# Kernel optimization log

Hardware: AMD Instinct MI355X
Metric: run time of the kernel (lower is better)

## Reference

```python
import jax, jax.numpy as jnp
import numpy as np

EPS = 1e-4  # matches torch: x.norm(2, dim=1, keepdim=True) + 0.0001

def setup_inputs() -> dict:
    key = jax.random.key(0)
    k1, k2, k3 = jax.random.split(key, 3)
    B, IN, OUT = 16384, 2048, 2048
    x = jax.random.normal(k1, (B, IN), dtype=jnp.float32)
    # nn.Linear default init: U(-1/sqrt(in), 1/sqrt(in))
    bound = 1.0 / np.sqrt(IN)
    W = jax.random.uniform(k2, (OUT, IN), dtype=jnp.float32, minval=-bound, maxval=bound)
    b = jax.random.uniform(k3, (OUT,), dtype=jnp.float32, minval=-bound, maxval=bound)
    return {"x": x, "W": W, "b": b}

def reference(x, W, b):
    # L2-normalize each row, then Linear, then ReLU
    norm = jnp.linalg.norm(x, ord=2, axis=1, keepdims=True)  # [B, 1]
    x_dir = x / (norm + EPS)
    h = jnp.einsum('bi,oi->bo', x_dir, W) + b  # [B, OUT]
    return jax.nn.relu(h)
```

## Files before the change

kernel.cpp:

```cpp
#include <hip/hip_runtime.h>
#include <hip/hip_bf16.h>
#include <stdint.h>

#define B_ROWS 16384
#define IN_DIM 2048
#define OUT_DIM 2048

typedef __attribute__((ext_vector_type(4))) float f32x4;
typedef __attribute__((ext_vector_type(8))) short s16x8;

__device__ __forceinline__ unsigned short f2bf_rne(float f) {
  union { float f; unsigned u; } c; c.f = f;
  unsigned u = c.u;
  return (unsigned short)((u + 0x7FFFu + ((u >> 16) & 1u)) >> 16);
}

__global__ void __launch_bounds__(256) prep_x_kernel(const float* __restrict__ x,
                                                     unsigned short* __restrict__ xn,
                                                     float* __restrict__ scale) {
  const int row = blockIdx.x;
  const int t = threadIdx.x;
  const float4* xr = (const float4*)(x + (size_t)row * IN_DIM);
  float4 v0 = xr[t * 2 + 0];
  float4 v1 = xr[t * 2 + 1];
  float ss = v0.x * v0.x + v0.y * v0.y + v0.z * v0.z + v0.w * v0.w +
             v1.x * v1.x + v1.y * v1.y + v1.z * v1.z + v1.w * v1.w;
  s16x8 p;
  p[0] = (short)f2bf_rne(v0.x); p[1] = (short)f2bf_rne(v0.y);
  p[2] = (short)f2bf_rne(v0.z); p[3] = (short)f2bf_rne(v0.w);
  p[4] = (short)f2bf_rne(v1.x); p[5] = (short)f2bf_rne(v1.y);
  p[6] = (short)f2bf_rne(v1.z); p[7] = (short)f2bf_rne(v1.w);
  *(s16x8*)(xn + (size_t)row * IN_DIM + t * 8) = p;

  #pragma unroll
  for (int off = 32; off > 0; off >>= 1) ss += __shfl_down(ss, off, 64);
  __shared__ float red[4];
  if ((t & 63) == 0) red[t >> 6] = ss;
  __syncthreads();
  if (t == 0) {
    float s = red[0] + red[1] + red[2] + red[3];
    scale[row] = 1.0f / (sqrtf(s) + 1e-4f);
  }
}

__global__ void __launch_bounds__(256) prep_w_kernel(const float* __restrict__ W,
                                                     unsigned short* __restrict__ Wb) {
  const size_t base = (size_t)blockIdx.x * 2048 + (size_t)threadIdx.x * 8;
  const float4* wp = (const float4*)(W + base);
  float4 v0 = wp[0];
  float4 v1 = wp[1];
  s16x8 p;
  p[0] = (short)f2bf_rne(v0.x); p[1] = (short)f2bf_rne(v0.y);
  p[2] = (short)f2bf_rne(v0.z); p[3] = (short)f2bf_rne(v0.w);
  p[4] = (short)f2bf_rne(v1.x); p[5] = (short)f2bf_rne(v1.y);
  p[6] = (short)f2bf_rne(v1.z); p[7] = (short)f2bf_rne(v1.w);
  *(s16x8*)(Wb + base) = p;
}

__global__ void __launch_bounds__(256) gemm_kernel(const unsigned short* __restrict__ A,
                                                   const unsigned short* __restrict__ Bm,
                                                   const float* __restrict__ scale,
                                                   const float* __restrict__ bias,
                                                   float* __restrict__ out) {
  constexpr int BK = 64;
  __shared__ short As[128 * BK];
  __shared__ short Bs[128 * BK];

  const int tid  = threadIdx.x;
  const int bn   = blockIdx.x;
  const int bm   = blockIdx.y;
  const int lane = tid & 63;
  const int wave = tid >> 6;
  const int wm   = wave >> 1;
  const int wn   = wave & 1;
  const int lrow = lane & 15;
  const int lq   = lane >> 4;

  const int ar = tid >> 3;
  const int ac = (tid & 7) * 8;
  const unsigned short* ag = A  + (size_t)(bm * 128 + ar) * IN_DIM + ac;
  const unsigned short* bg = Bm + (size_t)(bn * 128 + ar) * IN_DIM + ac;
  char* asl = (char*)As + tid * 16;
  char* bsl = (char*)Bs + tid * 16;

  f32x4 acc[4][4] = {};

  for (int k0 = 0; k0 < IN_DIM; k0 += BK) {
    #pragma unroll
    for (int i = 0; i < 4; ++i) {
      __builtin_amdgcn_global_load_lds(
          (const __attribute__((address_space(1))) unsigned int*)(ag + (size_t)i * 32 * IN_DIM),
          (__attribute__((address_space(3))) unsigned int*)(asl + i * 4096), 16, 0, 0);
    }
    #pragma unroll
    for (int i = 0; i < 4; ++i) {
      __builtin_amdgcn_global_load_lds(
          (const __attribute__((address_space(1))) unsigned int*)(bg + (size_t)i * 32 * IN_DIM),
          (__attribute__((address_space(3))) unsigned int*)(bsl + i * 4096), 16, 0, 0);
    }
    ag += BK;
    bg += BK;
    __syncthreads();

    #pragma unroll
    for (int kk = 0; kk < 2; ++kk) {
      s16x8 af[4], bf[4];
      #pragma unroll
      for (int mi = 0; mi < 4; ++mi)
        af[mi] = *(const s16x8*)(As + (wm * 64 + mi * 16 + lrow) * BK + kk * 32 + lq * 8);
      #pragma unroll
      for (int ni = 0; ni < 4; ++ni)
        bf[ni] = *(const s16x8*)(Bs + (wn * 64 + ni * 16 + lrow) * BK + kk * 32 + lq * 8);
      #pragma unroll
      for (int mi = 0; mi < 4; ++mi)
        #pragma unroll
        for (int ni = 0; ni < 4; ++ni)
          acc[mi][ni] = __builtin_amdgcn_mfma_f32_16x16x32_bf16(af[mi], bf[ni], acc[mi][ni], 0, 0, 0);
    }
    __syncthreads();
  }

  const int row0 = bm * 128 + wm * 64 + lq * 4;
  const int col0 = bn * 128 + wn * 64 + lrow;
  #pragma unroll
  for (int mi = 0; mi < 4; ++mi) {
    const int row = row0 + mi * 16;
    const f32x4 sc = *(const f32x4*)(scale + row);
    #pragma unroll
    for (int ni = 0; ni < 4; ++ni) {
      const int col = col0 + ni * 16;
      const float bcol = bias[col];
      #pragma unroll
      for (int r = 0; r < 4; ++r) {
        float v = acc[mi][ni][r] * sc[r] + bcol;
        out[(size_t)(row + r) * OUT_DIM + col] = fmaxf(v, 0.0f);
      }
    }
  }
}

extern "C" void kernel_launch(void* const* d_in, const int* in_sizes, int n_in,
                              void* d_out, int out_size, void* d_ws, size_t ws_size,
                              hipStream_t stream) {
  const float* x = (const float*)d_in[0];
  const float* W = (const float*)d_in[1];
  const float* b = (const float*)d_in[2];
  float* out = (float*)d_out;

  char* ws = (char*)d_ws;
  unsigned short* xn    = (unsigned short*)ws;
  unsigned short* Wb    = (unsigned short*)(ws + (size_t)67108864);
  float*          scale = (float*)(ws + (size_t)67108864 + (size_t)8388608);

  prep_x_kernel<<<B_ROWS, 256, 0, stream>>>(x, xn, scale);
  prep_w_kernel<<<(OUT_DIM * IN_DIM) / 2048, 256, 0, stream>>>(W, Wb);

  dim3 grid(OUT_DIM / 128, B_ROWS / 128);
  gemm_kernel<<<grid, 256, 0, stream>>>(xn, Wb, scale, b, out);
}
```

Before: 421.3 us.

## Swizzle GEMM LDS tiles with XOR and use one wave per row in x prep

The GEMM now loads global tiles into LDS with an XOR-swizzled column chunk (chunk index XOR row mod 8), and the MFMA fragment reads apply the same swizzle. This is meant to remove LDS bank conflicts, since sixteen lanes read the same column offset from rows spaced 128 bytes apart. The x-normalisation prep kernel also switches to one wavefront per row, processing four rows per block, so the reduction uses only shuffles with no shared memory or block barrier. The swizzle has to match exactly between the global-to-LDS write and the fragment reads, or results are silently wrong.

Measured after the change: 381.5 us. 9.4% less time.

```diff
diff --git a/kernel.cpp b/kernel.cpp
--- a/kernel.cpp
+++ b/kernel.cpp
@@ -18,29 +18,30 @@
 __global__ void __launch_bounds__(256) prep_x_kernel(const float* __restrict__ x,
                                                      unsigned short* __restrict__ xn,
                                                      float* __restrict__ scale) {
-  const int row = blockIdx.x;
-  const int t = threadIdx.x;
+  const int row  = (blockIdx.x * 256 + threadIdx.x) >> 6;
+  const int lane = threadIdx.x & 63;
   const float4* xr = (const float4*)(x + (size_t)row * IN_DIM);
-  float4 v0 = xr[t * 2 + 0];
-  float4 v1 = xr[t * 2 + 1];
-  float ss = v0.x * v0.x + v0.y * v0.y + v0.z * v0.z + v0.w * v0.w +
-             v1.x * v1.x + v1.y * v1.y + v1.z * v1.z + v1.w * v1.w;
-  s16x8 p;
-  p[0] = (short)f2bf_rne(v0.x); p[1] = (short)f2bf_rne(v0.y);
-  p[2] = (short)f2bf_rne(v0.z); p[3] = (short)f2bf_rne(v0.w);
-  p[4] = (short)f2bf_rne(v1.x); p[5] = (short)f2bf_rne(v1.y);
-  p[6] = (short)f2bf_rne(v1.z); p[7] = (short)f2bf_rne(v1.w);
-  *(s16x8*)(xn + (size_t)row * IN_DIM + t * 8) = p;
+  unsigned short* xrow = xn + (size_t)row * IN_DIM;
+
+  float ss = 0.0f;
+  #pragma unroll
+  for (int j = 0; j < 4; ++j) {
+    const int f4 = j * 128 + lane * 2;
+    float4 v0 = xr[f4 + 0];
+    float4 v1 = xr[f4 + 1];
+    ss += v0.x * v0.x + v0.y * v0.y + v0.z * v0.z + v0.w * v0.w +
+          v1.x * v1.x + v1.y * v1.y + v1.z * v1.z + v1.w * v1.w;
+    s16x8 p;
+    p[0] = (short)f2bf_rne(v0.x); p[1] = (short)f2bf_rne(v0.y);
+    p[2] = (short)f2bf_rne(v0.z); p[3] = (short)f2bf_rne(v0.w);
+    p[4] = (short)f2bf_rne(v1.x); p[5] = (short)f2bf_rne(v1.y);
+    p[6] = (short)f2bf_rne(v1.z); p[7] = (short)f2bf_rne(v1.w);
+    *(s16x8*)(xrow + f4 * 4) = p;
+  }
 
   #pragma unroll
-  for (int off = 32; off > 0; off >>= 1) ss += __shfl_down(ss, off, 64);
-  __shared__ float red[4];
-  if ((t & 63) == 0) red[t >> 6] = ss;
-  __syncthreads();
-  if (t == 0) {
-    float s = red[0] + red[1] + red[2] + red[3];
-    scale[row] = 1.0f / (sqrtf(s) + 1e-4f);
-  }
+  for (int m = 32; m > 0; m >>= 1) ss += __shfl_xor(ss, m, 64);
+  if (lane == 0) scale[row] = 1.0f / (sqrtf(ss) + 1e-4f);
 }
 
 __global__ void __launch_bounds__(256) prep_w_kernel(const float* __restrict__ W,
@@ -77,7 +78,7 @@
   const int lq   = lane >> 4;
 
   const int ar = tid >> 3;
-  const int ac = (tid & 7) * 8;
+  const int ac = ((tid & 7) ^ (ar & 7)) * 8;
   const unsigned short* ag = A  + (size_t)(bm * 128 + ar) * IN_DIM + ac;
   const unsigned short* bg = Bm + (size_t)(bn * 128 + ar) * IN_DIM + ac;
   char* asl = (char*)As + tid * 16;
@@ -106,11 +107,15 @@
     for (int kk = 0; kk < 2; ++kk) {
       s16x8 af[4], bf[4];
       #pragma unroll
-      for (int mi = 0; mi < 4; ++mi)
-        af[mi] = *(const s16x8*)(As + (wm * 64 + mi * 16 + lrow) * BK + kk * 32 + lq * 8);
+      for (int mi = 0; mi < 4; ++mi) {
+        const int R = wm * 64 + mi * 16 + lrow;
+        af[mi] = *(const s16x8*)(As + R * BK + (((kk * 4 + lq) ^ (lrow & 7)) * 8));
+      }
       #pragma unroll
-      for (int ni = 0; ni < 4; ++ni)
-        bf[ni] = *(const s16x8*)(Bs + (wn * 64 + ni * 16 + lrow) * BK + kk * 32 + lq * 8);
+      for (int ni = 0; ni < 4; ++ni) {
+        const int R = wn * 64 + ni * 16 + lrow;
+        bf[ni] = *(const s16x8*)(Bs + R * BK + (((kk * 4 + lq) ^ (lrow & 7)) * 8));
+      }
       #pragma unroll
       for (int mi = 0; mi < 4; ++mi)
         #pragma unroll
@@ -152,7 +157,7 @@
   unsigned short* Wb    = (unsigned short*)(ws + (size_t)67108864);
   float*          scale = (float*)(ws + (size_t)67108864 + (size_t)8388608);
 
-  prep_x_kernel<<<B_ROWS, 256, 0, stream>>>(x, xn, scale);
+  prep_x_kernel<<<B_ROWS / 4, 256, 0, stream>>>(x, xn, scale);
   prep_w_kernel<<<(OUT_DIM * IN_DIM) / 2048, 256, 0, stream>>>(W, Wb);
 
   dim3 grid(OUT_DIM / 128, B_ROWS / 128);
```
